# Performance work log

Hardware: AMD Instinct MI355X
Metric: run time of the kernel (lower is better)

The kernel has to match this reference:

```python
import jax, jax.numpy as jnp
import numpy as np


def setup_inputs() -> dict:
    key = jax.random.key(0)
    k1, k2 = jax.random.split(key)
    embedding = jax.random.normal(k1, (8192, 256), dtype=jnp.float32)
    label = jax.random.randint(k2, (8192,), 0, 1000, dtype=jnp.int64 if jax.config.jax_enable_x64 else jnp.int32)
    return {"embedding": embedding, "label": label}


def reference(embedding, label):
    # embedding: [B, W]; label is unused by the original module's math.
    B, W = embedding.shape
    miu = embedding.mean(axis=0)                      # [W]
    ec = embedding - miu                              # [B, W] centered
    # mean over batch of outer products ec[b] ec[b]^T == (ec^T @ ec) / B
    cov = jnp.einsum('bi,bj->ij', ec, ec) / B         # [W, W]
    diff = cov - jnp.eye(W, dtype=embedding.dtype)
    loss = jnp.sqrt(jnp.sum(diff * diff))             # Frobenius norm
    return loss
```

## Files before the change

kernel.cpp:

```cpp
#include <hip/hip_runtime.h>
#include <math.h>

typedef unsigned int uint32;
typedef unsigned short u16;
typedef __bf16 bf16x8 __attribute__((ext_vector_type(8)));
typedef float f32x16 __attribute__((ext_vector_type(16)));
typedef float f32x4  __attribute__((ext_vector_type(4)));

#define BROWS 8192
#define WDIM 256
#define NT 3
#define CHUNKS 64
#define RPB 128
#define TILE_ELEMS 16384
#define GRID_BLKS (NT * CHUNKS)

#define WS_CSB_U16 (CHUNKS * NT * TILE_ELEMS)
#define WS_LOSS_F32 1581056

__device__ unsigned g_done = 0;
__device__ unsigned g_fin  = 0;

__device__ __forceinline__ uint32 pack2bf(float lo, float hi) {
    uint32 a = __float_as_uint(lo), b = __float_as_uint(hi);
    a = (a + 0x7FFFu + ((a >> 16) & 1u)) >> 16;
    b = (b + 0x7FFFu + ((b >> 16) & 1u)) >> 16;
    return (a & 0xFFFFu) | (b << 16);
}
__device__ __forceinline__ uint32 f2bf(float x) {
    uint32 a = __float_as_uint(x);
    return (a + 0x7FFFu + ((a >> 16) & 1u)) >> 16;
}
__device__ __forceinline__ float bflo(uint32 v) { return __uint_as_float(v << 16); }
__device__ __forceinline__ float bfhi(uint32 v) { return __uint_as_float(v & 0xFFFF0000u); }
__device__ __forceinline__ float bf(u16 v) { return __uint_as_float(((uint32)v) << 16); }

__device__ __forceinline__ int uswz(int col, int krp) {
    return col * 64 + ((((krp >> 2) ^ (col & 15)) << 2) | (krp & 3));
}

__device__ __forceinline__ void aputf(float* p, float v) {
    __hip_atomic_store(p, v, __ATOMIC_RELAXED, __HIP_MEMORY_SCOPE_AGENT);
}
__device__ __forceinline__ void aput16(u16* p, uint32 v) {
    asm volatile("global_store_short %0, %1, off sc0 sc1"
                 :: "v"(p), "v"(v) : "memory");
}

#define LD8(R0,R1,R2,R3,R4,R5,R6,R7,P0,P1,P2,P3,P4,P5,P6,P7)                 \
    asm volatile(                                                            \
        "global_load_dwordx4 %0, %8, off sc0 sc1\n\t"                        \
        "global_load_dwordx4 %1, %9, off sc0 sc1\n\t"                        \
        "global_load_dwordx4 %2, %10, off sc0 sc1\n\t"                       \
        "global_load_dwordx4 %3, %11, off sc0 sc1\n\t"                       \
        "global_load_dwordx4 %4, %12, off sc0 sc1\n\t"                       \
        "global_load_dwordx4 %5, %13, off sc0 sc1\n\t"                       \
        "global_load_dwordx4 %6, %14, off sc0 sc1\n\t"                       \
        "global_load_dwordx4 %7, %15, off sc0 sc1\n\t"                       \
        "s_waitcnt vmcnt(0)"                                                 \
        : "=&v"(R0),"=&v"(R1),"=&v"(R2),"=&v"(R3),                           \
          "=&v"(R4),"=&v"(R5),"=&v"(R6),"=&v"(R7)                            \
        : "v"(P0),"v"(P1),"v"(P2),"v"(P3),                                   \
          "v"(P4),"v"(P5),"v"(P6),"v"(P7))

#define LD1(R0,P0)                                                           \
    asm volatile("global_load_dwordx4 %0, %1, off sc0 sc1\n\t"               \
                 "s_waitcnt vmcnt(0)" : "=&v"(R0) : "v"(P0))

__global__ __launch_bounds__(256)
void corr_onepass(const float* __restrict__ E, float* __restrict__ ws,
                  float* __restrict__ out) {
    __shared__ uint32 U[WDIM * 64];
    __shared__ float red[4];
    __shared__ int amFinal;
    const int t = blockIdx.x, c = blockIdx.y;
    const int tid = threadIdx.x;
    const int bid = c * NT + t;

    const int ncg = (t == 1) ? 4 : 2;
    const int gcol0 = (t == 2) ? 128 : 0;
    const int row0 = c * RPB;
    const int c4 = tid & 15, rp = tid >> 4;
    const int w = tid >> 6, l = tid & 63, lm = l & 31;
    const int bBase = (t == 1) ? 128 : 0;
    const int colA = w * 32 + lm;

#define ISSUE(CG, FA, FB) do {                                                 \
    const float* Eb_ = E + (size_t)row0 * WDIM + gcol0 + (CG) * 64;            \
    _Pragma("unroll")                                                          \
    for (int p = 0; p < 4; ++p) {                                              \
        const int r0_ = 2 * (rp + 16 * p);                                     \
        FA[p] = *(const float4*)(Eb_ + (size_t)r0_ * WDIM + c4 * 4);           \
        FB[p] = *(const float4*)(Eb_ + (size_t)(r0_ + 1) * WDIM + c4 * 4);     \
    }                                                                          \
} while (0)

#define WRITE(CG, FA, FB) do {                                                 \
    const int colb_ = (CG) * 64 + c4 * 4;                                      \
    _Pragma("unroll")                                                          \
    for (int p = 0; p < 4; ++p) {                                              \
        const int krp_ = rp + 16 * p;                                          \
        U[uswz(colb_ + 0, krp_)] = pack2bf(FA[p].x, FB[p].x);                  \
        U[uswz(colb_ + 1, krp_)] = pack2bf(FA[p].y, FB[p].y);                  \
        U[uswz(colb_ + 2, krp_)] = pack2bf(FA[p].z, FB[p].z);                  \
        U[uswz(colb_ + 3, krp_)] = pack2bf(FA[p].w, FB[p].w);                  \
    }                                                                          \
} while (0)

    float4 Afa[4], Afb[4], Bfa[4], Bfb[4];
    ISSUE(0, Afa, Afb);
    for (int it = 0; it < ncg; it += 2) {
        ISSUE(it + 1, Bfa, Bfb);
        WRITE(it, Afa, Afb);
        if (it + 2 < ncg) ISSUE(it + 2, Afa, Afb);
        WRITE(it + 1, Bfa, Bfb);
    }
    __syncthreads();

    float csum = 0.f;
    if (t == 1) {
        #pragma unroll
        for (int g = 0; g < 16; ++g) {
            const uint4 v = *(const uint4*)&U[tid * 64 + ((g ^ (tid & 15)) << 2)];
            csum += bflo(v.x) + bfhi(v.x) + bflo(v.y) + bfhi(v.y)
                  + bflo(v.z) + bfhi(v.z) + bflo(v.w) + bfhi(v.w);
        }
    }

    f32x16 acc[4];
    #pragma unroll
    for (int n = 0; n < 4; ++n)
        #pragma unroll
        for (int r = 0; r < 16; ++r) acc[n][r] = 0.f;

    #pragma unroll
    for (int s8 = 0; s8 < 8; ++s8) {
        const int grp = 2 * s8 + (l >> 5);
        const bf16x8 a = *(const bf16x8*)&U[colA * 64 + ((grp ^ (colA & 15)) << 2)];
        #pragma unroll
        for (int n = 0; n < 4; ++n) {
            const int colB = bBase + n * 32 + lm;
            const bf16x8 b = *(const bf16x8*)&U[colB * 64 + ((grp ^ (colB & 15)) << 2)];
            acc[n] = __builtin_amdgcn_mfma_f32_32x32x16_bf16(a, b, acc[n], 0, 0, 0);
        }
    }

    u16* part = (u16*)ws;
    u16* dst = part + ((size_t)bid) * TILE_ELEMS;
    const int rbase = 32 * w + 4 * (l >> 5);
    #pragma unroll
    for (int n = 0; n < 4; ++n)
        #pragma unroll
        for (int r = 0; r < 16; ++r) {
            const int row = rbase + (r & 3) + 8 * (r >> 2);
            aput16(&dst[row * 128 + n * 32 + lm], f2bf(acc[n][r]));
        }
    if (t == 1) aput16(&part[WS_CSB_U16 + c * WDIM + tid], f2bf(csum));

    asm volatile("s_waitcnt vmcnt(0)" ::: "memory");
    __syncthreads();
    if (tid == 0) {
        const unsigned d = __hip_atomic_fetch_add(
            &g_done, 1u, __ATOMIC_RELAXED, __HIP_MEMORY_SCOPE_AGENT);
        const unsigned target = d - (d % GRID_BLKS) + GRID_BLKS;
        while (__hip_atomic_load(&g_done, __ATOMIC_RELAXED,
                                 __HIP_MEMORY_SCOPE_AGENT) < target)
            __builtin_amdgcn_s_sleep(4);
    }
    __syncthreads();

    const int e0 = bid * 256;
    const int tt = e0 >> 14, local0 = e0 & 16383;
    const int h = l >> 5, q = l & 31;
    const int cc0 = w * 16 + h * 8;
    const u16* baseG = part + (size_t)tt * TILE_ELEMS + local0 + 8 * q;
    const u16* baseM = part + WS_CSB_U16 + 8 * q;

    uint4 g0, g1, g2, g3, g4, g5, g6, g7;
    uint4 m0, m1, m2, m3, m4, m5, m6, m7;
    LD8(g0, g1, g2, g3, g4, g5, g6, g7,
        (const uint4*)(baseG + (size_t)(cc0 + 0) * (NT * TILE_ELEMS)),
        (const uint4*)(baseG + (size_t)(cc0 + 1) * (NT * TILE_ELEMS)),
        (const uint4*)(baseG + (size_t)(cc0 + 2) * (NT * TILE_ELEMS)),
        (const uint4*)(baseG + (size_t)(cc0 + 3) * (NT * TILE_ELEMS)),
        (const uint4*)(baseG + (size_t)(cc0 + 4) * (NT * TILE_ELEMS)),
        (const uint4*)(baseG + (size_t)(cc0 + 5) * (NT * TILE_ELEMS)),
        (const uint4*)(baseG + (size_t)(cc0 + 6) * (NT * TILE_ELEMS)),
        (const uint4*)(baseG + (size_t)(cc0 + 7) * (NT * TILE_ELEMS)));
    LD8(m0, m1, m2, m3, m4, m5, m6, m7,
        (const uint4*)(baseM + (cc0 + 0) * WDIM),
        (const uint4*)(baseM + (cc0 + 1) * WDIM),
        (const uint4*)(baseM + (cc0 + 2) * WDIM),
        (const uint4*)(baseM + (cc0 + 3) * WDIM),
        (const uint4*)(baseM + (cc0 + 4) * WDIM),
        (const uint4*)(baseM + (cc0 + 5) * WDIM),
        (const uint4*)(baseM + (cc0 + 6) * WDIM),
        (const uint4*)(baseM + (cc0 + 7) * WDIM));

    float gs[8] = {0,0,0,0,0,0,0,0}, ms[8] = {0,0,0,0,0,0,0,0};
#define ACC8(S, V) do {                                                      \
    S[0] += bflo(V.x); S[1] += bfhi(V.x); S[2] += bflo(V.y); S[3] += bfhi(V.y);\
    S[4] += bflo(V.z); S[5] += bfhi(V.z); S[6] += bflo(V.w); S[7] += bfhi(V.w);\
} while (0)
    ACC8(gs, g0); ACC8(gs, g1); ACC8(gs, g2); ACC8(gs, g3);
    ACC8(gs, g4); ACC8(gs, g5); ACC8(gs, g6); ACC8(gs, g7);
    ACC8(ms, m0); ACC8(ms, m1); ACC8(ms, m2); ACC8(ms, m3);
    ACC8(ms, m4); ACC8(ms, m5); ACC8(ms, m6); ACC8(ms, m7);

    float* redg = (float*)U;
    float* redm = redg + 2048;
    float* muS  = redg + 4096;
    const int grpi = w * 2 + h;
    #pragma unroll
    for (int j2 = 0; j2 < 8; ++j2) {
        redg[grpi * 256 + 8 * q + j2] = gs[j2];
        redm[grpi * 256 + 8 * q + j2] = ms[j2];
    }
    __syncthreads();
    {
        float s = 0.f;
        #pragma unroll
        for (int gg = 0; gg < 8; ++gg) s += redm[gg * 256 + tid];
        muS[tid] = s * (1.0f / (float)BROWS);
    }
    float gsum = 0.f;
    #pragma unroll
    for (int gg = 0; gg < 8; ++gg) gsum += redg[gg * 256 + tid];
    __syncthreads();

    const int local = local0 + tid;
    const int i = ((tt == 2) ? 128 : 0) + (local >> 7);
    const int j = ((tt == 0) ? 0 : 128) + (local & 127);
    const float diff = gsum * (1.0f / (float)BROWS) - muS[i] * muS[j]
                     - ((i == j) ? 1.0f : 0.0f);
    float v = ((tt == 1) ? 2.0f : 1.0f) * diff * diff;

    #pragma unroll
    for (int o = 32; o > 0; o >>= 1) v += __shfl_down(v, o, 64);
    if ((tid & 63) == 0) red[tid >> 6] = v;
    __syncthreads();

    float* lossp = ws + WS_LOSS_F32;
    if (tid == 0) aputf(&lossp[bid], red[0] + red[1] + red[2] + red[3]);
    asm volatile("s_waitcnt vmcnt(0)" ::: "memory");
    __syncthreads();
    if (tid == 0) {
        const unsigned d2 = __hip_atomic_fetch_add(
            &g_fin, 1u, __ATOMIC_RELAXED, __HIP_MEMORY_SCOPE_AGENT);
        amFinal = ((d2 % GRID_BLKS) == GRID_BLKS - 1);
    }
    __syncthreads();
    if (!amFinal) return;

    f32x4 lv4 = {0.f, 0.f, 0.f, 0.f};
    if (tid < 48) LD1(lv4, (const f32x4*)(lossp + 4 * tid));
    if (tid < 64) {
        float lv = lv4[0] + lv4[1] + lv4[2] + lv4[3];
        #pragma unroll
        for (int o = 32; o > 0; o >>= 1) lv += __shfl_down(lv, o, 64);
        if (tid == 0) out[0] = sqrtf(lv);
    }
}

extern "C" void kernel_launch(void* const* d_in, const int* in_sizes, int n_in,
                              void* d_out, int out_size, void* d_ws, size_t ws_size,
                              hipStream_t stream) {
    const float* E = (const float*)d_in[0];
    float* out = (float*)d_out;
    float* ws = (float*)d_ws;

    corr_onepass<<<dim3(NT, CHUNKS), 256, 0, stream>>>(E, ws, out);
}
```

Measured before the change: 72.97 us.

## Merge three tile blocks per row chunk into one 512-thread block

Replaces the 3x64 grid of 256-thread blocks, each loading part of a 128-row chunk and computing one 128x128 Gram tile, with 64 blocks of 512 threads that load the full chunk once and compute all three tiles. This removes the duplicate global loads and bf16 staging of the same rows across blocks, and shrinks the grid barrier and final reduction to 64 participants. In exchange it runs fewer, larger blocks, which lowers parallelism on a GPU with many CUs. The post-barrier reduction is also restructured into two phases per block.

```diff
diff --git a/kernel.cpp b/kernel.cpp
--- a/kernel.cpp
+++ b/kernel.cpp
@@ -13,7 +13,7 @@
 #define CHUNKS 64
 #define RPB 128
 #define TILE_ELEMS 16384
-#define GRID_BLKS (NT * CHUNKS)
+#define GRID_BLKS 64
 
 #define WS_CSB_U16 (CHUNKS * NT * TILE_ELEMS)
 #define WS_LOSS_F32 1581056
@@ -33,7 +33,6 @@
 }
 __device__ __forceinline__ float bflo(uint32 v) { return __uint_as_float(v << 16); }
 __device__ __forceinline__ float bfhi(uint32 v) { return __uint_as_float(v & 0xFFFF0000u); }
-__device__ __forceinline__ float bf(u16 v) { return __uint_as_float(((uint32)v) << 16); }
 
 __device__ __forceinline__ int uswz(int col, int krp) {
     return col * 64 + ((((krp >> 2) ^ (col & 15)) << 2) | (krp & 3));
@@ -67,29 +66,29 @@
     asm volatile("global_load_dwordx4 %0, %1, off sc0 sc1\n\t"               \
                  "s_waitcnt vmcnt(0)" : "=&v"(R0) : "v"(P0))
 
-__global__ __launch_bounds__(256)
-void corr_onepass(const float* __restrict__ E, float* __restrict__ ws,
-                  float* __restrict__ out) {
+#define ACC8(S, V) do {                                                      \
+    S[0] += bflo(V.x); S[1] += bfhi(V.x); S[2] += bflo(V.y); S[3] += bfhi(V.y);\
+    S[4] += bflo(V.z); S[5] += bfhi(V.z); S[6] += bflo(V.w); S[7] += bfhi(V.w);\
+} while (0)
+
+__global__ __launch_bounds__(512)
+void corr_v8(const float* __restrict__ E, float* __restrict__ ws,
+             float* __restrict__ out) {
     __shared__ uint32 U[WDIM * 64];
-    __shared__ float red[4];
+    __shared__ float red[8];
     __shared__ int amFinal;
-    const int t = blockIdx.x, c = blockIdx.y;
+    const int c = blockIdx.x;
     const int tid = threadIdx.x;
-    const int bid = c * NT + t;
-
-    const int ncg = (t == 1) ? 4 : 2;
-    const int gcol0 = (t == 2) ? 128 : 0;
+    u16* part = (u16*)ws;
+
     const int row0 = c * RPB;
     const int c4 = tid & 15, rp = tid >> 4;
-    const int w = tid >> 6, l = tid & 63, lm = l & 31;
-    const int bBase = (t == 1) ? 128 : 0;
-    const int colA = w * 32 + lm;
 
 #define ISSUE(CG, FA, FB) do {                                                 \
-    const float* Eb_ = E + (size_t)row0 * WDIM + gcol0 + (CG) * 64;            \
+    const float* Eb_ = E + (size_t)row0 * WDIM + (CG) * 64;                    \
     _Pragma("unroll")                                                          \
-    for (int p = 0; p < 4; ++p) {                                              \
-        const int r0_ = 2 * (rp + 16 * p);                                     \
+    for (int p = 0; p < 2; ++p) {                                              \
+        const int r0_ = 2 * (rp + 32 * p);                                     \
         FA[p] = *(const float4*)(Eb_ + (size_t)r0_ * WDIM + c4 * 4);           \
         FB[p] = *(const float4*)(Eb_ + (size_t)(r0_ + 1) * WDIM + c4 * 4);     \
     }                                                                          \
@@ -98,8 +97,8 @@
 #define WRITE(CG, FA, FB) do {                                                 \
     const int colb_ = (CG) * 64 + c4 * 4;                                      \
     _Pragma("unroll")                                                          \
-    for (int p = 0; p < 4; ++p) {                                              \
-        const int krp_ = rp + 16 * p;                                          \
+    for (int p = 0; p < 2; ++p) {                                              \
+        const int krp_ = rp + 32 * p;                                          \
         U[uswz(colb_ + 0, krp_)] = pack2bf(FA[p].x, FB[p].x);                  \
         U[uswz(colb_ + 1, krp_)] = pack2bf(FA[p].y, FB[p].y);                  \
         U[uswz(colb_ + 2, krp_)] = pack2bf(FA[p].z, FB[p].z);                  \
@@ -107,18 +106,18 @@
     }                                                                          \
 } while (0)
 
-    float4 Afa[4], Afb[4], Bfa[4], Bfb[4];
+    float4 Afa[2], Afb[2], Bfa[2], Bfb[2];
     ISSUE(0, Afa, Afb);
-    for (int it = 0; it < ncg; it += 2) {
+    for (int it = 0; it < 4; it += 2) {
         ISSUE(it + 1, Bfa, Bfb);
         WRITE(it, Afa, Afb);
-        if (it + 2 < ncg) ISSUE(it + 2, Afa, Afb);
+        if (it + 2 < 4) ISSUE(it + 2, Afa, Afb);
         WRITE(it + 1, Bfa, Bfb);
     }
     __syncthreads();
 
     float csum = 0.f;
-    if (t == 1) {
+    if (tid < 256) {
         #pragma unroll
         for (int g = 0; g < 16; ++g) {
             const uint4 v = *(const uint4*)&U[tid * 64 + ((g ^ (tid & 15)) << 2)];
@@ -127,35 +126,62 @@
         }
     }
 
-    f32x16 acc[4];
+    const int w8 = tid >> 6, l = tid & 63, lm = l & 31;
+    const int rg = w8 & 3;
+    const bool hiW = (w8 >= 4);
+    const int colA2 = rg * 32 + lm;
+    const int colA1 = (hiW ? 128 : 0) + rg * 32 + lm;
+    const int bOff = hiW ? 128 : 0;
+    const int t1n0 = hiW ? 2 : 0;
+
+    f32x16 accA[4], accB[2];
     #pragma unroll
     for (int n = 0; n < 4; ++n)
         #pragma unroll
-        for (int r = 0; r < 16; ++r) acc[n][r] = 0.f;
-
+        for (int r = 0; r < 16; ++r) accA[n][r] = 0.f;
+    #pragma unroll
+    for (int m = 0; m < 2; ++m)
+        #pragma unroll
+        for (int r = 0; r < 16; ++r) accB[m][r] = 0.f;
+
+#define FRAG(COL) (*(const bf16x8*)&U[(COL) * 64 + ((grp ^ ((COL) & 15)) << 2)])
     #pragma unroll
     for (int s8 = 0; s8 < 8; ++s8) {
         const int grp = 2 * s8 + (l >> 5);
-        const bf16x8 a = *(const bf16x8*)&U[colA * 64 + ((grp ^ (colA & 15)) << 2)];
+        const bf16x8 aL = FRAG(colA2);
+        bf16x8 aM;
+        if (hiW) aM = FRAG(colA1); else aM = aL;
         #pragma unroll
         for (int n = 0; n < 4; ++n) {
-            const int colB = bBase + n * 32 + lm;
-            const bf16x8 b = *(const bf16x8*)&U[colB * 64 + ((grp ^ (colB & 15)) << 2)];
-            acc[n] = __builtin_amdgcn_mfma_f32_32x32x16_bf16(a, b, acc[n], 0, 0, 0);
-        }
-    }
-
-    u16* part = (u16*)ws;
-    u16* dst = part + ((size_t)bid) * TILE_ELEMS;
-    const int rbase = 32 * w + 4 * (l >> 5);
+            const bf16x8 b = FRAG(bOff + n * 32 + lm);
+            accA[n] = __builtin_amdgcn_mfma_f32_32x32x16_bf16(aM, b, accA[n], 0, 0, 0);
+        }
+        #pragma unroll
+        for (int m = 0; m < 2; ++m) {
+            const bf16x8 b = FRAG(128 + (t1n0 + m) * 32 + lm);
+            accB[m] = __builtin_amdgcn_mfma_f32_32x32x16_bf16(aL, b, accB[m], 0, 0, 0);
+        }
+    }
+
+    const int tMain = hiW ? 2 : 0;
+    u16* dstM = part + (size_t)(c * NT + tMain) * TILE_ELEMS;
+    u16* dst1 = part + (size_t)(c * NT + 1) * TILE_ELEMS;
+    const int rbase = 32 * rg + 4 * (l >> 5);
     #pragma unroll
     for (int n = 0; n < 4; ++n)
         #pragma unroll
         for (int r = 0; r < 16; ++r) {
             const int row = rbase + (r & 3) + 8 * (r >> 2);
-            aput16(&dst[row * 128 + n * 32 + lm], f2bf(acc[n][r]));
-        }
-    if (t == 1) aput16(&part[WS_CSB_U16 + c * WDIM + tid], f2bf(csum));
+            aput16(&dstM[row * 128 + n * 32 + lm], f2bf(accA[n][r]));
+        }
+    #pragma unroll
+    for (int m = 0; m < 2; ++m)
+        #pragma unroll
+        for (int r = 0; r < 16; ++r) {
+            const int row = rbase + (r & 3) + 8 * (r >> 2);
+            aput16(&dst1[row * 128 + (t1n0 + m) * 32 + lm], f2bf(accB[m][r]));
+        }
+    if (tid < 256) aput16(&part[WS_CSB_U16 + c * WDIM + tid], f2bf(csum));
 
     asm volatile("s_waitcnt vmcnt(0)" ::: "memory");
     __syncthreads();
@@ -169,79 +195,121 @@
     }
     __syncthreads();
 
-    const int e0 = bid * 256;
-    const int tt = e0 >> 14, local0 = e0 & 16383;
-    const int h = l >> 5, q = l & 31;
-    const int cc0 = w * 16 + h * 8;
-    const u16* baseG = part + (size_t)tt * TILE_ELEMS + local0 + 8 * q;
-    const u16* baseM = part + WS_CSB_U16 + 8 * q;
-
-    uint4 g0, g1, g2, g3, g4, g5, g6, g7;
-    uint4 m0, m1, m2, m3, m4, m5, m6, m7;
-    LD8(g0, g1, g2, g3, g4, g5, g6, g7,
-        (const uint4*)(baseG + (size_t)(cc0 + 0) * (NT * TILE_ELEMS)),
-        (const uint4*)(baseG + (size_t)(cc0 + 1) * (NT * TILE_ELEMS)),
-        (const uint4*)(baseG + (size_t)(cc0 + 2) * (NT * TILE_ELEMS)),
-        (const uint4*)(baseG + (size_t)(cc0 + 3) * (NT * TILE_ELEMS)),
-        (const uint4*)(baseG + (size_t)(cc0 + 4) * (NT * TILE_ELEMS)),
-        (const uint4*)(baseG + (size_t)(cc0 + 5) * (NT * TILE_ELEMS)),
-        (const uint4*)(baseG + (size_t)(cc0 + 6) * (NT * TILE_ELEMS)),
-        (const uint4*)(baseG + (size_t)(cc0 + 7) * (NT * TILE_ELEMS)));
-    LD8(m0, m1, m2, m3, m4, m5, m6, m7,
-        (const uint4*)(baseM + (cc0 + 0) * WDIM),
-        (const uint4*)(baseM + (cc0 + 1) * WDIM),
-        (const uint4*)(baseM + (cc0 + 2) * WDIM),
-        (const uint4*)(baseM + (cc0 + 3) * WDIM),
-        (const uint4*)(baseM + (cc0 + 4) * WDIM),
-        (const uint4*)(baseM + (cc0 + 5) * WDIM),
-        (const uint4*)(baseM + (cc0 + 6) * WDIM),
-        (const uint4*)(baseM + (cc0 + 7) * WDIM));
-
-    float gs[8] = {0,0,0,0,0,0,0,0}, ms[8] = {0,0,0,0,0,0,0,0};
-#define ACC8(S, V) do {                                                      \
-    S[0] += bflo(V.x); S[1] += bfhi(V.x); S[2] += bflo(V.y); S[3] += bfhi(V.y);\
-    S[4] += bflo(V.z); S[5] += bfhi(V.z); S[6] += bflo(V.w); S[7] += bfhi(V.w);\
-} while (0)
-    ACC8(gs, g0); ACC8(gs, g1); ACC8(gs, g2); ACC8(gs, g3);
-    ACC8(gs, g4); ACC8(gs, g5); ACC8(gs, g6); ACC8(gs, g7);
-    ACC8(ms, m0); ACC8(ms, m1); ACC8(ms, m2); ACC8(ms, m3);
-    ACC8(ms, m4); ACC8(ms, m5); ACC8(ms, m6); ACC8(ms, m7);
-
-    float* redg = (float*)U;
-    float* redm = redg + 2048;
-    float* muS  = redg + 4096;
-    const int grpi = w * 2 + h;
-    #pragma unroll
-    for (int j2 = 0; j2 < 8; ++j2) {
-        redg[grpi * 256 + 8 * q + j2] = gs[j2];
-        redm[grpi * 256 + 8 * q + j2] = ms[j2];
-    }
-    __syncthreads();
+    float* muS   = (float*)U;
+    float* redm  = (float*)U + 256;
+    float* redgA = (float*)U + 2304;
+    float* redgB = (float*)U + 4352;
+    const int local0 = c * 256;
+
+    if (tid < 256) {
+        const int l2 = tid & 63, w2 = tid >> 6, h2 = l2 >> 5, q2 = l2 & 31;
+        const int cc0 = w2 * 16 + h2 * 8, grpi = w2 * 2 + h2;
+        const u16* baseM = part + WS_CSB_U16 + 8 * q2;
+        uint4 m0, m1, m2, m3, m4, m5, m6, m7;
+        LD8(m0, m1, m2, m3, m4, m5, m6, m7,
+            (const uint4*)(baseM + (cc0 + 0) * WDIM),
+            (const uint4*)(baseM + (cc0 + 1) * WDIM),
+            (const uint4*)(baseM + (cc0 + 2) * WDIM),
+            (const uint4*)(baseM + (cc0 + 3) * WDIM),
+            (const uint4*)(baseM + (cc0 + 4) * WDIM),
+            (const uint4*)(baseM + (cc0 + 5) * WDIM),
+            (const uint4*)(baseM + (cc0 + 6) * WDIM),
+            (const uint4*)(baseM + (cc0 + 7) * WDIM));
+        float ms[8] = {0,0,0,0,0,0,0,0};
+        ACC8(ms, m0); ACC8(ms, m1); ACC8(ms, m2); ACC8(ms, m3);
+        ACC8(ms, m4); ACC8(ms, m5); ACC8(ms, m6); ACC8(ms, m7);
+        #pragma unroll
+        for (int j2 = 0; j2 < 8; ++j2) redm[grpi * 256 + 8 * q2 + j2] = ms[j2];
+    }
+
+    const int hh = tid >> 8, tl = tid & 255;
+    const int l3 = tl & 63, w3 = tl >> 6, h3 = l3 >> 5, q3 = l3 & 31;
+    const int cc0g = w3 * 16 + h3 * 8, grpg = w3 * 2 + h3;
     {
+        const u16* baseG = part + (size_t)hh * TILE_ELEMS + local0 + 8 * q3;
+        uint4 g0, g1, g2, g3, g4, g5, g6, g7;
+        LD8(g0, g1, g2, g3, g4, g5, g6, g7,
+            (const uint4*)(baseG + (size_t)(cc0g + 0) * (NT * TILE_ELEMS)),
+            (const uint4*)(baseG + (size_t)(cc0g + 1) * (NT * TILE_ELEMS)),
+            (const uint4*)(baseG + (size_t)(cc0g + 2) * (NT * TILE_ELEMS)),
+            (const uint4*)(baseG + (size_t)(cc0g + 3) * (NT * TILE_ELEMS)),
+            (const uint4*)(baseG + (size_t)(cc0g + 4) * (NT * TILE_ELEMS)),
+            (const uint4*)(baseG + (size_t)(cc0g + 5) * (NT * TILE_ELEMS)),
+            (const uint4*)(baseG + (size_t)(cc0g + 6) * (NT * TILE_ELEMS)),
+            (const uint4*)(baseG + (size_t)(cc0g + 7) * (NT * TILE_ELEMS)));
+        float gs[8] = {0,0,0,0,0,0,0,0};
+        ACC8(gs, g0); ACC8(gs, g1); ACC8(gs, g2); ACC8(gs, g3);
+        ACC8(gs, g4); ACC8(gs, g5); ACC8(gs, g6); ACC8(gs, g7);
+        float* rgp = hh ? redgB : redgA;
+        #pragma unroll
+        for (int j2 = 0; j2 < 8; ++j2) rgp[grpg * 256 + 8 * q3 + j2] = gs[j2];
+    }
+    __syncthreads();
+    if (tid < 256) {
         float s = 0.f;
         #pragma unroll
         for (int gg = 0; gg < 8; ++gg) s += redm[gg * 256 + tid];
         muS[tid] = s * (1.0f / (float)BROWS);
     }
-    float gsum = 0.f;
-    #pragma unroll
-    for (int gg = 0; gg < 8; ++gg) gsum += redg[gg * 256 + tid];
-    __syncthreads();
-
-    const int local = local0 + tid;
-    const int i = ((tt == 2) ? 128 : 0) + (local >> 7);
-    const int j = ((tt == 0) ? 0 : 128) + (local & 127);
-    const float diff = gsum * (1.0f / (float)BROWS) - muS[i] * muS[j]
-                     - ((i == j) ? 1.0f : 0.0f);
-    float v = ((tt == 1) ? 2.0f : 1.0f) * diff * diff;
+    __syncthreads();
+
+    float v = 0.f;
+    {
+        const float* rgp = hh ? redgB : redgA;
+        float gsum = 0.f;
+        #pragma unroll
+        for (int gg = 0; gg < 8; ++gg) gsum += rgp[gg * 256 + tl];
+        const int local = local0 + tl;
+        const int i = ((hh == 0) ? 0 : 0) + (local >> 7);
+        const int j = ((hh == 0) ? 0 : 128) + (local & 127);
+        const float diff = gsum * (1.0f / (float)BROWS) - muS[i] * muS[j]
+                         - ((i == j) ? 1.0f : 0.0f);
+        v += ((hh == 1) ? 2.0f : 1.0f) * diff * diff;
+    }
+    __syncthreads();
+
+    if (tid < 256) {
+        const u16* baseG = part + (size_t)2 * TILE_ELEMS + local0 + 8 * q3;
+        uint4 g0, g1, g2, g3, g4, g5, g6, g7;
+        LD8(g0, g1, g2, g3, g4, g5, g6, g7,
+            (const uint4*)(baseG + (size_t)(cc0g + 0) * (NT * TILE_ELEMS)),
+            (const uint4*)(baseG + (size_t)(cc0g + 1) * (NT * TILE_ELEMS)),
+            (const uint4*)(baseG + (size_t)(cc0g + 2) * (NT * TILE_ELEMS)),
+            (const uint4*)(baseG + (size_t)(cc0g + 3) * (NT * TILE_ELEMS)),
+            (const uint4*)(baseG + (size_t)(cc0g + 4) * (NT * TILE_ELEMS)),
+            (const uint4*)(baseG + (size_t)(cc0g + 5) * (NT * TILE_ELEMS)),
+            (const uint4*)(baseG + (size_t)(cc0g + 6) * (NT * TILE_ELEMS)),
+            (const uint4*)(baseG + (size_t)(cc0g + 7) * (NT * TILE_ELEMS)));
+        float gs[8] = {0,0,0,0,0,0,0,0};
+        ACC8(gs, g0); ACC8(gs, g1); ACC8(gs, g2); ACC8(gs, g3);
+        ACC8(gs, g4); ACC8(gs, g5); ACC8(gs, g6); ACC8(gs, g7);
+        #pragma unroll
+        for (int j2 = 0; j2 < 8; ++j2) redgA[grpg * 256 + 8 * q3 + j2] = gs[j2];
+    }
+    __syncthreads();
+    if (tid < 256) {
+        float gsum = 0.f;
+        #pragma unroll
+        for (int gg = 0; gg < 8; ++gg) gsum += redgA[gg * 256 + tid];
+        const int local = local0 + tid;
+        const int i = 128 + (local >> 7);
+        const int j = 128 + (local & 127);
+        const float diff = gsum * (1.0f / (float)BROWS) - muS[i] * muS[j]
+                         - ((i == j) ? 1.0f : 0.0f);
+        v += diff * diff;
+    }
 
     #pragma unroll
     for (int o = 32; o > 0; o >>= 1) v += __shfl_down(v, o, 64);
     if ((tid & 63) == 0) red[tid >> 6] = v;
     __syncthreads();
-
     float* lossp = ws + WS_LOSS_F32;
-    if (tid == 0) aputf(&lossp[bid], red[0] + red[1] + red[2] + red[3]);
+    if (tid == 0) {
+        float bl = 0.f;
+        #pragma unroll
+        for (int k = 0; k < 8; ++k) bl += red[k];
+        aputf(&lossp[c], bl);
+    }
     asm volatile("s_waitcnt vmcnt(0)" ::: "memory");
     __syncthreads();
     if (tid == 0) {
@@ -253,7 +321,7 @@
     if (!amFinal) return;
 
     f32x4 lv4 = {0.f, 0.f, 0.f, 0.f};
-    if (tid < 48) LD1(lv4, (const f32x4*)(lossp + 4 * tid));
+    if (tid < 16) LD1(lv4, (const f32x4*)(lossp + 4 * tid));
     if (tid < 64) {
         float lv = lv4[0] + lv4[1] + lv4[2] + lv4[3];
         #pragma unroll
@@ -269,5 +337,5 @@
     float* out = (float*)d_out;
     float* ws = (float*)d_ws;
 
-    corr_onepass<<<dim3(NT, CHUNKS), 256, 0, stream>>>(E, ws, out);
-}
+    corr_v8<<<dim3(GRID_BLKS), 512, 0, stream>>>(E, ws, out);
+}
```

Measured after the change: 72.25 us. About the same (-1.0%).
